# Kernel optimization log

Measured on AMD Instinct MI355X. Metric: run time of the kernel, lower is better.

## Reference

```python
import jax, jax.numpy as jnp
import numpy as np
import math

MAX_FREQ = 3
OMEGA = 0.5 * math.pi
C = (2 * MAX_FREQ + 1) ** 2  # 49
SQRT2 = math.sqrt(2.0)


def setup_inputs() -> dict:
    key = jax.random.key(0)
    N = 2_000_000
    x = jax.random.normal(key, (N, 3 * C + 2), dtype=jnp.float32)
    return {"x": x}


def _embed(v):
    # v: [N] scalar coordinate -> [N, 2*max_freq+1]
    # order matches torch: [1, sqrt2*cos(1w), sqrt2*sin(1w), cos(2w), sin(2w), ...]
    t = v * OMEGA
    freqs = jnp.arange(1, MAX_FREQ + 1, dtype=t.dtype)  # [F]
    tf = t[:, None] * freqs  # [N, F]
    cs = jnp.stack([SQRT2 * jnp.cos(tf), SQRT2 * jnp.sin(tf)], axis=-1)  # [N, F, 2]
    inter = cs.reshape(v.shape[0], -1)  # [N, 2F] interleaved cos/sin
    ones = jnp.ones((v.shape[0], 1), dtype=t.dtype)
    return jnp.concatenate([ones, inter], axis=-1)  # [N, 2F+1]


def reference(x):
    x = x.reshape(-1, x.shape[-1])  # [N, 3c+2]
    rel = x[:, -2:]
    latent = x[:, :-2]  # [N, 3c]
    N = x.shape[0]
    X = _embed(rel[:, 0])  # [N, 7]
    Y = _embed(rel[:, 1])  # [N, 7]
    # outer product X^T Y flattened row-major over (x_dim, y_dim) -> [N, 49]
    ope_flat = (X[:, :, None] * Y[:, None, :]).reshape(N, -1)
    lat = latent.reshape(N, 3, C)  # channels R,G,B contiguous in torch layout
    out = jnp.einsum('nc,nkc->nk', ope_flat, lat)  # [N, 3]
    return out / 100.0
```

## Files before the change

kernel.cpp:

```cpp
#include <hip/hip_runtime.h>
#include <math.h>


#define RL    149
#define ROWS  64
#define BLOCK 256
#define NK    3

__global__ __launch_bounds__(BLOCK)
void ope_kernel(const float* __restrict__ x, float* __restrict__ out, int nrows) {
    __shared__ float tile[ROWS * RL];
    __shared__ float outs[ROWS * NK];

    const int tid = threadIdx.x;
    const long long row0 = (long long)blockIdx.x * ROWS;
    int vr = nrows - (int)row0;
    if (vr > ROWS) vr = ROWS;
    const int nflt = vr * RL;
    const float* __restrict__ src = x + row0 * RL;

    if ((nflt & 3) == 0) {
        const float4* s4 = (const float4*)src;
        float4* d4 = (float4*)tile;
        const int n4 = nflt >> 2;
        for (int i = tid; i < n4; i += BLOCK) d4[i] = s4[i];
    } else {
        for (int i = tid; i < nflt; i += BLOCK) tile[i] = src[i];
    }
    __syncthreads();

    if (tid < vr) {
        const float* __restrict__ row = tile + tid * RL;
        const float OMEGA = 1.5707963267948966f;
        const float S2    = 1.4142135623730951f;
        const float t0 = row[147] * OMEGA;
        const float t1 = row[148] * OMEGA;
        float X[7], Y[7];
        X[0] = 1.f; Y[0] = 1.f;
        #pragma unroll
        for (int f = 1; f <= 3; ++f) {
            float s, c;
            __sincosf(t0 * (float)f, &s, &c);
            X[2*f-1] = S2 * c;
            X[2*f]   = S2 * s;
            __sincosf(t1 * (float)f, &s, &c);
            Y[2*f-1] = S2 * c;
            Y[2*f]   = S2 * s;
        }
        float acc0 = 0.f, acc1 = 0.f, acc2 = 0.f;
        #pragma unroll
        for (int i = 0; i < 7; ++i) {
            #pragma unroll
            for (int j = 0; j < 7; ++j) {
                const float p = X[i] * Y[j];
                const int c = i * 7 + j;
                acc0 = fmaf(p, row[c],      acc0);
                acc1 = fmaf(p, row[49 + c], acc1);
                acc2 = fmaf(p, row[98 + c], acc2);
            }
        }
        outs[tid * 3 + 0] = acc0 * 0.01f;
        outs[tid * 3 + 1] = acc1 * 0.01f;
        outs[tid * 3 + 2] = acc2 * 0.01f;
    }
    __syncthreads();

    const int nout = vr * NK;
    float* __restrict__ dst = out + row0 * NK;
    for (int i = tid; i < nout; i += BLOCK) dst[i] = outs[i];
}

extern "C" void kernel_launch(void* const* d_in, const int* in_sizes, int n_in,
                              void* d_out, int out_size, void* d_ws, size_t ws_size,
                              hipStream_t stream) {
    const float* x = (const float*)d_in[0];
    float* out = (float*)d_out;
    const int nrows = in_sizes[0] / RL;
    const int grid = (nrows + ROWS - 1) / ROWS;
    ope_kernel<<<grid, BLOCK, 0, stream>>>(x, out, nrows);
}
```

Measured before the change: 262.2 us.

## Use persistent single-wave blocks with double-buffered direct global-to-LDS loads

Replaces the one-tile-per-block kernel with a persistent grid of single-wavefront blocks. Each block walks over tiles, using global_load_lds to copy the next 64-row tile straight into LDS while it computes on the current one, and waits on explicit vmcnt counts. Outputs are written directly from registers instead of going through a shared staging buffer. This aims to overlap memory traffic with compute and drop block-wide syncs and register round-trips, at the cost of relying on exact outstanding-load counts and low occupancy per block. Leftover rows beyond full tiles are handled by block 0 reading straight from global memory.

```diff
diff --git a/kernel.cpp b/kernel.cpp
--- a/kernel.cpp
+++ b/kernel.cpp
@@ -1,73 +1,97 @@
 #include <hip/hip_runtime.h>
+#include <stdint.h>
 #include <math.h>
 
 
-#define RL    149
-#define ROWS  64
-#define BLOCK 256
-#define NK    3
+#define RL      149
+#define RTILE   64
+#define TILE_B  (RTILE * RL * 4)
+#define FULLCH  37
+#define OVOFF   (TILE_B - 1024)
+#define GRID    2048
+#define NK      3
 
-__global__ __launch_bounds__(BLOCK)
+typedef const __attribute__((address_space(1))) unsigned int as1_uint;
+typedef __attribute__((address_space(3))) unsigned int as3_uint;
+
+__device__ __forceinline__ void stage_tile(const char* __restrict__ src,
+                                           char* dst, int lane) {
+    #pragma unroll
+    for (int ci = 0; ci < FULLCH; ++ci)
+        __builtin_amdgcn_global_load_lds((as1_uint*)(src + ci * 1024 + lane * 16),
+                                         (as3_uint*)(dst + ci * 1024), 16, 0, 0);
+    __builtin_amdgcn_global_load_lds((as1_uint*)(src + OVOFF + lane * 16),
+                                     (as3_uint*)(dst + OVOFF), 16, 0, 0);
+}
+
+__device__ __forceinline__ void compute_row(const float* __restrict__ row,
+                                            float* __restrict__ dst) {
+    const float OMEGA = 1.5707963267948966f;
+    const float S2    = 1.4142135623730951f;
+    const float t0 = row[147] * OMEGA;
+    const float t1 = row[148] * OMEGA;
+    float X[7], Y[7];
+    X[0] = 1.f; Y[0] = 1.f;
+    #pragma unroll
+    for (int f = 1; f <= 3; ++f) {
+        float s, c;
+        __sincosf(t0 * (float)f, &s, &c);
+        X[2*f-1] = S2 * c; X[2*f] = S2 * s;
+        __sincosf(t1 * (float)f, &s, &c);
+        Y[2*f-1] = S2 * c; Y[2*f] = S2 * s;
+    }
+    float a0 = 0.f, a1 = 0.f, a2 = 0.f;
+    #pragma unroll
+    for (int i = 0; i < 7; ++i)
+        #pragma unroll
+        for (int j = 0; j < 7; ++j) {
+            const float p = X[i] * Y[j];
+            const int c = i * 7 + j;
+            a0 = fmaf(p, row[c],      a0);
+            a1 = fmaf(p, row[49 + c], a1);
+            a2 = fmaf(p, row[98 + c], a2);
+        }
+    dst[0] = a0 * 0.01f; dst[1] = a1 * 0.01f; dst[2] = a2 * 0.01f;
+}
+
+__global__ __launch_bounds__(64)
 void ope_kernel(const float* __restrict__ x, float* __restrict__ out, int nrows) {
-    __shared__ float tile[ROWS * RL];
-    __shared__ float outs[ROWS * NK];
+    __shared__ __align__(16) char lds[2 * TILE_B];
+    const int lane = threadIdx.x;
+    const char* __restrict__ xb = (const char*)x;
+    const int ntile = nrows / RTILE;
+    const long long tfirst = blockIdx.x;
+    const int GW = gridDim.x;
 
-    const int tid = threadIdx.x;
-    const long long row0 = (long long)blockIdx.x * ROWS;
-    int vr = nrows - (int)row0;
-    if (vr > ROWS) vr = ROWS;
-    const int nflt = vr * RL;
-    const float* __restrict__ src = x + row0 * RL;
+    if (tfirst < ntile) stage_tile(xb + tfirst * TILE_B, lds, lane);
 
-    if ((nflt & 3) == 0) {
-        const float4* s4 = (const float4*)src;
-        float4* d4 = (float4*)tile;
-        const int n4 = nflt >> 2;
-        for (int i = tid; i < n4; i += BLOCK) d4[i] = s4[i];
-    } else {
-        for (int i = tid; i < nflt; i += BLOCK) tile[i] = src[i];
+    int p = 0;
+    for (long long t = tfirst; t < ntile; t += GW, p ^= 1) {
+        const long long tn = t + GW;
+        if (tn < ntile) {
+            stage_tile(xb + tn * TILE_B, lds + (p ^ 1) * TILE_B, lane);
+            asm volatile("s_waitcnt vmcnt(38)" ::: "memory");
+        } else {
+            asm volatile("s_waitcnt vmcnt(0)" ::: "memory");
+        }
+        __builtin_amdgcn_sched_barrier(0);
+
+        const float* row = (const float*)(lds + p * TILE_B) + lane * RL;
+        float o[NK];
+        compute_row(row, o);
+        float* __restrict__ dst = out + (t * RTILE + lane) * NK;
+        dst[0] = o[0]; dst[1] = o[1]; dst[2] = o[2];
     }
-    __syncthreads();
 
-    if (tid < vr) {
-        const float* __restrict__ row = tile + tid * RL;
-        const float OMEGA = 1.5707963267948966f;
-        const float S2    = 1.4142135623730951f;
-        const float t0 = row[147] * OMEGA;
-        const float t1 = row[148] * OMEGA;
-        float X[7], Y[7];
-        X[0] = 1.f; Y[0] = 1.f;
-        #pragma unroll
-        for (int f = 1; f <= 3; ++f) {
-            float s, c;
-            __sincosf(t0 * (float)f, &s, &c);
-            X[2*f-1] = S2 * c;
-            X[2*f]   = S2 * s;
-            __sincosf(t1 * (float)f, &s, &c);
-            Y[2*f-1] = S2 * c;
-            Y[2*f]   = S2 * s;
+    if (blockIdx.x == 0) {
+        for (int r = ntile * RTILE + lane; r < nrows; r += 64) {
+            const float* row = x + (long long)r * RL;
+            float o[NK];
+            compute_row(row, o);
+            float* dst = out + (long long)r * NK;
+            dst[0] = o[0]; dst[1] = o[1]; dst[2] = o[2];
         }
-        float acc0 = 0.f, acc1 = 0.f, acc2 = 0.f;
-        #pragma unroll
-        for (int i = 0; i < 7; ++i) {
-            #pragma unroll
-            for (int j = 0; j < 7; ++j) {
-                const float p = X[i] * Y[j];
-                const int c = i * 7 + j;
-                acc0 = fmaf(p, row[c],      acc0);
-                acc1 = fmaf(p, row[49 + c], acc1);
-                acc2 = fmaf(p, row[98 + c], acc2);
-            }
-        }
-        outs[tid * 3 + 0] = acc0 * 0.01f;
-        outs[tid * 3 + 1] = acc1 * 0.01f;
-        outs[tid * 3 + 2] = acc2 * 0.01f;
     }
-    __syncthreads();
-
-    const int nout = vr * NK;
-    float* __restrict__ dst = out + row0 * NK;
-    for (int i = tid; i < nout; i += BLOCK) dst[i] = outs[i];
 }
 
 extern "C" void kernel_launch(void* const* d_in, const int* in_sizes, int n_in,
@@ -76,6 +100,5 @@
     const float* x = (const float*)d_in[0];
     float* out = (float*)d_out;
     const int nrows = in_sizes[0] / RL;
-    const int grid = (nrows + ROWS - 1) / ROWS;
-    ope_kernel<<<grid, BLOCK, 0, stream>>>(x, out, nrows);
+    ope_kernel<<<GRID, 64, 0, stream>>>(x, out, nrows);
 }
```

Result: faster. 223.4 us (-14.8%).
